# Kernel tuning notes

Measured on AMD Instinct MI355X. Metric: run time of the kernel, lower is better.

Reference implementation:

```python
import jax, jax.numpy as jnp
import numpy as np

LMBDA = 0.1
ALPHA = 0.05
NBIT = 4


def setup_inputs() -> dict:
    key = jax.random.key(0)
    k1, k2 = jax.random.split(key)
    shape = (4096, 16384)
    weight = jax.random.normal(k1, shape, dtype=jnp.float32) * 0.05
    Qn, Qp = -2 ** (NBIT - 1), 2 ** (NBIT - 1) - 1
    q_int = jax.random.randint(k2, shape, Qn, Qp + 1)  # bins in [-8, 7]
    weight_q = (q_int.astype(jnp.float32)) * ALPHA
    alpha = jnp.full((1,), ALPHA, dtype=jnp.float32)
    return {"weight": weight, "weight_q": weight_q, "nbit": NBIT, "alpha": alpha}


def reference(weight, weight_q, nbit, alpha):
    # dampening_loss with aggregation='mean', scaled by lmbda (single quant layer)
    Qn = -2 ** (nbit - 1)
    Qp = 2 ** (nbit - 1) - 1
    nbins = Qp - Qn + 1
    a = alpha.reshape(())

    # (w_q.detach() - w)^2 mean  (detach is a no-op in fwd)
    loss = jnp.mean((weight_q - weight) ** 2)

    # Fused histogram pass: per-bin count / sum / sumsq of `weight`,
    # keyed by the quant bin of weight_q (exact-equality mask in original).
    bin_id = jnp.round(weight_q / a).astype(jnp.int32) - Qn  # [0, nbins)
    w = weight.reshape(-1)
    b = bin_id.reshape(-1)
    cnt = jax.ops.segment_sum(jnp.ones_like(w), b, num_segments=nbins)
    s = jax.ops.segment_sum(w, b, num_segments=nbins)
    ss = jax.ops.segment_sum(w * w, b, num_segments=nbins)

    # unbiased variance per bin, only added when count > 1 (as in torch.var)
    denom_n = jnp.maximum(cnt, 1.0)
    denom_nm1 = jnp.maximum(cnt - 1.0, 1.0)
    var = (ss - s * s / denom_n) / denom_nm1
    loss = loss + jnp.sum(jnp.where(cnt > 1.0, var, 0.0))

    return LMBDA * loss
```

## Files before the change

kernel.cpp:

```cpp
#include <hip/hip_runtime.h>

#define NBINS  16
#define TPB    256
#define BLOCKS 768
#define PLANE  (NBINS * TPB)


__global__ __launch_bounds__(TPB) void binreg_main(
    const float* __restrict__ w, const float* __restrict__ wq,
    const float* __restrict__ alpha_p, const int* __restrict__ nbit_p,
    float* __restrict__ partial, long long n)
{
    __shared__ float  c_pl [PLANE];
    __shared__ float2 sv_pl[PLANE];
    __shared__ float  sqpart[TPB / 64];

    const int tid = threadIdx.x;

    #pragma unroll
    for (int k = 0; k < NBINS; ++k) {
        c_pl [k * TPB + tid] = 0.0f;
        sv_pl[k * TPB + tid] = make_float2(0.0f, 0.0f);
    }

    const float inv_a = 1.0f / alpha_p[0];
    const int   qoff  = 1 << (nbit_p[0] - 1);

    const long long n4     = n >> 2;
    const long long stride = (long long)BLOCKS * TPB;
    const float4* w4 = (const float4*)w;
    const float4* q4 = (const float4*)wq;

    float sq = 0.0f;

    for (long long i = (long long)blockIdx.x * TPB + tid; i < n4; i += stride) {
        float4 a = w4[i];
        float4 b = q4[i];

        float d0 = b.x - a.x, d1 = b.y - a.y, d2 = b.z - a.z, d3 = b.w - a.w;
        sq += d0 * d0 + d1 * d1 + d2 * d2 + d3 * d3;

        int i0 = ((((int)rintf(b.x * inv_a) + qoff) & (NBINS - 1)) << 8) + tid;
        int i1 = ((((int)rintf(b.y * inv_a) + qoff) & (NBINS - 1)) << 8) + tid;
        int i2 = ((((int)rintf(b.z * inv_a) + qoff) & (NBINS - 1)) << 8) + tid;
        int i3 = ((((int)rintf(b.w * inv_a) + qoff) & (NBINS - 1)) << 8) + tid;

        { c_pl[i0] += 1.0f; float2 t = sv_pl[i0]; t.x += a.x; t.y += a.x * a.x; sv_pl[i0] = t; }
        { c_pl[i1] += 1.0f; float2 t = sv_pl[i1]; t.x += a.y; t.y += a.y * a.y; sv_pl[i1] = t; }
        { c_pl[i2] += 1.0f; float2 t = sv_pl[i2]; t.x += a.z; t.y += a.z * a.z; sv_pl[i2] = t; }
        { c_pl[i3] += 1.0f; float2 t = sv_pl[i3]; t.x += a.w; t.y += a.w * a.w; sv_pl[i3] = t; }
    }

    for (long long i = (n4 << 2) + (long long)blockIdx.x * TPB + tid; i < n; i += stride) {
        float a = w[i], b = wq[i];
        float d = b - a;
        sq += d * d;
        int ii = ((((int)rintf(b * inv_a) + qoff) & (NBINS - 1)) << 8) + tid;
        c_pl[ii] += 1.0f; float2 t = sv_pl[ii]; t.x += a; t.y += a * a; sv_pl[ii] = t;
    }

    for (int off = 32; off; off >>= 1) sq += __shfl_down(sq, off, 64);
    const int wave = tid >> 6, lane = tid & 63;
    if (lane == 0) sqpart[wave] = sq;
    __syncthreads();

    for (int c = wave; c < 48; c += 4) {
        const int bin = c & 15;
        float v = 0.0f;
        if (c < 16) {
            #pragma unroll
            for (int r = 0; r < TPB / 64; ++r)
                v += c_pl[(bin << 8) + r * 64 + lane];
        } else if (c < 32) {
            #pragma unroll
            for (int r = 0; r < TPB / 64; ++r)
                v += sv_pl[(bin << 8) + r * 64 + lane].x;
        } else {
            #pragma unroll
            for (int r = 0; r < TPB / 64; ++r)
                v += sv_pl[(bin << 8) + r * 64 + lane].y;
        }
        for (int off = 32; off; off >>= 1) v += __shfl_down(v, off, 64);
        if (lane == 0) partial[c * BLOCKS + blockIdx.x] = v;
    }
    if (tid == 0)
        partial[48 * BLOCKS + blockIdx.x] =
            sqpart[0] + sqpart[1] + sqpart[2] + sqpart[3];
}

__global__ __launch_bounds__(TPB) void binreg_final(
    const float* __restrict__ partial, float* __restrict__ out, long long n)
{
    __shared__ float cell[49];
    const int tid = threadIdx.x, wave = tid >> 6, lane = tid & 63;

    for (int c = wave; c < 49; c += 4) {
        float v0 = 0.0f, v1 = 0.0f, v2 = 0.0f, v3 = 0.0f;
        for (int r = lane; r < BLOCKS; r += 256) {
            v0 += partial[c * BLOCKS + r];
            v1 += partial[c * BLOCKS + r + 64];
            v2 += partial[c * BLOCKS + r + 128];
            v3 += partial[c * BLOCKS + r + 192];
        }
        float v = (v0 + v1) + (v2 + v3);
        for (int off = 32; off; off >>= 1) v += __shfl_down(v, off, 64);
        if (lane == 0) cell[c] = v;
    }
    __syncthreads();

    if (tid == 0) {
        float loss = cell[48] / (float)n;
        #pragma unroll
        for (int b = 0; b < NBINS; ++b) {
            float cnt = cell[b];
            float s   = cell[16 + b];
            float ss  = cell[32 + b];
            if (cnt > 1.0f)
                loss += (ss - s * s / cnt) / (cnt - 1.0f);
        }
        out[0] = 0.1f * loss;
    }
}

extern "C" void kernel_launch(void* const* d_in, const int* in_sizes, int n_in,
                              void* d_out, int out_size, void* d_ws, size_t ws_size,
                              hipStream_t stream)
{
    const float* w     = (const float*)d_in[0];
    const float* wq    = (const float*)d_in[1];
    const int*   nbit  = (const int*)d_in[2];
    const float* alpha = (const float*)d_in[3];
    float* out     = (float*)d_out;
    float* partial = (float*)d_ws;
    long long n = (long long)in_sizes[0];

    binreg_main<<<BLOCKS, TPB, 0, stream>>>(w, wq, alpha, nbit, partial, n);
    binreg_final<<<1, TPB, 0, stream>>>(partial, out, n);
}
```

Measured before the change: 519.1 us.

## Count bins in packed register counters and merge duplicate bins before LDS updates

Per-bin counts move from a shared-memory plane into two 64-bit registers holding eight 8-bit counters each. These are flushed to float accumulators every 32 iterations and reduced across waves by shuffles. Within each float4, lanes that fall in the same bin are combined first, and duplicates are sent to a dummy LDS plane, so the four read-modify-writes never alias. The change also prefetches the next iteration's loads, raises the block count and adds an occupancy hint. It trades more VALU work and register pressure for less LDS traffic and shared-memory footprint.

```diff
diff --git a/kernel.cpp b/kernel.cpp
--- a/kernel.cpp
+++ b/kernel.cpp
@@ -2,26 +2,24 @@
 
 #define NBINS  16
 #define TPB    256
-#define BLOCKS 768
-#define PLANE  (NBINS * TPB)
-
-
-__global__ __launch_bounds__(TPB) void binreg_main(
+#define BLOCKS 1024
+#define DUMMY  16
+
+
+__global__ __launch_bounds__(TPB, 4) void binreg_main(
     const float* __restrict__ w, const float* __restrict__ wq,
     const float* __restrict__ alpha_p, const int* __restrict__ nbit_p,
     float* __restrict__ partial, long long n)
 {
-    __shared__ float  c_pl [PLANE];
-    __shared__ float2 sv_pl[PLANE];
+    __shared__ float2 sv_pl[(NBINS + 1) * TPB];
+    __shared__ float  cred[NBINS][TPB / 64];
     __shared__ float  sqpart[TPB / 64];
 
     const int tid = threadIdx.x;
 
     #pragma unroll
-    for (int k = 0; k < NBINS; ++k) {
-        c_pl [k * TPB + tid] = 0.0f;
+    for (int k = 0; k < NBINS; ++k)
         sv_pl[k * TPB + tid] = make_float2(0.0f, 0.0f);
-    }
 
     const float inv_a = 1.0f / alpha_p[0];
     const int   qoff  = 1 << (nbit_p[0] - 1);
@@ -32,46 +30,127 @@
     const float4* q4 = (const float4*)wq;
 
     float sq = 0.0f;
-
-    for (long long i = (long long)blockIdx.x * TPB + tid; i < n4; i += stride) {
+    unsigned long long clo = 0ull, chi = 0ull;
+    float cf[NBINS];
+    #pragma unroll
+    for (int k = 0; k < NBINS; ++k) cf[k] = 0.0f;
+    int pend = 0;
+
+    long long i = (long long)blockIdx.x * TPB + tid;
+    if (i < n4) {
         float4 a = w4[i];
         float4 b = q4[i];
-
-        float d0 = b.x - a.x, d1 = b.y - a.y, d2 = b.z - a.z, d3 = b.w - a.w;
-        sq += d0 * d0 + d1 * d1 + d2 * d2 + d3 * d3;
-
-        int i0 = ((((int)rintf(b.x * inv_a) + qoff) & (NBINS - 1)) << 8) + tid;
-        int i1 = ((((int)rintf(b.y * inv_a) + qoff) & (NBINS - 1)) << 8) + tid;
-        int i2 = ((((int)rintf(b.z * inv_a) + qoff) & (NBINS - 1)) << 8) + tid;
-        int i3 = ((((int)rintf(b.w * inv_a) + qoff) & (NBINS - 1)) << 8) + tid;
-
-        { c_pl[i0] += 1.0f; float2 t = sv_pl[i0]; t.x += a.x; t.y += a.x * a.x; sv_pl[i0] = t; }
-        { c_pl[i1] += 1.0f; float2 t = sv_pl[i1]; t.x += a.y; t.y += a.y * a.y; sv_pl[i1] = t; }
-        { c_pl[i2] += 1.0f; float2 t = sv_pl[i2]; t.x += a.z; t.y += a.z * a.z; sv_pl[i2] = t; }
-        { c_pl[i3] += 1.0f; float2 t = sv_pl[i3]; t.x += a.w; t.y += a.w * a.w; sv_pl[i3] = t; }
-    }
-
-    for (long long i = (n4 << 2) + (long long)blockIdx.x * TPB + tid; i < n; i += stride) {
-        float a = w[i], b = wq[i];
-        float d = b - a;
+        for (;;) {
+            const long long in  = i + stride;
+            const bool     more = in < n4;
+            float4 an, bn;
+            if (more) { an = w4[in]; bn = q4[in]; }
+
+            float d0 = b.x - a.x, d1 = b.y - a.y, d2 = b.z - a.z, d3 = b.w - a.w;
+            sq += d0 * d0 + d1 * d1 + d2 * d2 + d3 * d3;
+
+            const int b0 = (((int)rintf(b.x * inv_a)) + qoff) & (NBINS - 1);
+            const int b1 = (((int)rintf(b.y * inv_a)) + qoff) & (NBINS - 1);
+            const int b2 = (((int)rintf(b.z * inv_a)) + qoff) & (NBINS - 1);
+            const int b3 = (((int)rintf(b.w * inv_a)) + qoff) & (NBINS - 1);
+
+            {
+                unsigned long long t;
+                t = 1ull << ((b0 & 7) << 3); clo += (b0 < 8) ? t : 0ull; chi += (b0 < 8) ? 0ull : t;
+                t = 1ull << ((b1 & 7) << 3); clo += (b1 < 8) ? t : 0ull; chi += (b1 < 8) ? 0ull : t;
+                t = 1ull << ((b2 & 7) << 3); clo += (b2 < 8) ? t : 0ull; chi += (b2 < 8) ? 0ull : t;
+                t = 1ull << ((b3 & 7) << 3); clo += (b3 < 8) ? t : 0ull; chi += (b3 < 8) ? 0ull : t;
+            }
+
+            const bool e10 = (b1 == b0);
+            const bool e20 = (b2 == b0);
+            const bool e21 = (b2 == b1) && !e20;
+            const bool e30 = (b3 == b0);
+            const bool e31 = (b3 == b1) && !e30;
+            const bool e32 = (b3 == b2) && !e30 && !e31;
+
+            float sx0 = a.x, sx1 = a.y, sx2 = a.z, sx3 = a.w;
+            float qx0 = a.x * a.x, qx1 = a.y * a.y, qx2 = a.z * a.z, qx3 = a.w * a.w;
+
+            sx0 += e10 ? sx1 : 0.0f;  qx0 += e10 ? qx1 : 0.0f;
+            sx0 += e20 ? sx2 : 0.0f;  qx0 += e20 ? qx2 : 0.0f;
+            sx1 += e21 ? sx2 : 0.0f;  qx1 += e21 ? qx2 : 0.0f;
+            sx0 += e30 ? sx3 : 0.0f;  qx0 += e30 ? qx3 : 0.0f;
+            sx1 += e31 ? sx3 : 0.0f;  qx1 += e31 ? qx3 : 0.0f;
+            sx2 += e32 ? sx3 : 0.0f;  qx2 += e32 ? qx3 : 0.0f;
+
+            const int r1 = e10               ? DUMMY : b1;
+            const int r2 = (e20 | e21)       ? DUMMY : b2;
+            const int r3 = (e30 | e31 | e32) ? DUMMY : b3;
+            const int a0 = (b0 << 8) + tid;
+            const int a1 = (r1 << 8) + tid;
+            const int a2 = (r2 << 8) + tid;
+            const int a3 = (r3 << 8) + tid;
+
+            float2 t0 = sv_pl[a0];
+            float2 t1 = sv_pl[a1];
+            float2 t2 = sv_pl[a2];
+            float2 t3 = sv_pl[a3];
+            t0.x += sx0; t0.y += qx0;
+            t1.x += sx1; t1.y += qx1;
+            t2.x += sx2; t2.y += qx2;
+            t3.x += sx3; t3.y += qx3;
+            sv_pl[a0] = t0;
+            sv_pl[a1] = t1;
+            sv_pl[a2] = t2;
+            sv_pl[a3] = t3;
+
+            if (++pend >= 32) {
+                #pragma unroll
+                for (int k = 0; k < 8; ++k) {
+                    cf[k]     += (float)((clo >> (k * 8)) & 0xffull);
+                    cf[k + 8] += (float)((chi >> (k * 8)) & 0xffull);
+                }
+                clo = 0ull; chi = 0ull; pend = 0;
+            }
+
+            if (!more) break;
+            a = an; b = bn; i = in;
+        }
+    }
+
+    for (long long t = (n4 << 2) + (long long)blockIdx.x * TPB + tid; t < n; t += stride) {
+        float av = w[t], bv = wq[t];
+        float d = bv - av;
         sq += d * d;
-        int ii = ((((int)rintf(b * inv_a) + qoff) & (NBINS - 1)) << 8) + tid;
-        c_pl[ii] += 1.0f; float2 t = sv_pl[ii]; t.x += a; t.y += a * a; sv_pl[ii] = t;
+        int bb = (((int)rintf(bv * inv_a)) + qoff) & (NBINS - 1);
+        unsigned long long one = 1ull << ((bb & 7) << 3);
+        clo += (bb < 8) ? one : 0ull; chi += (bb < 8) ? 0ull : one;
+        int aa = (bb << 8) + tid;
+        float2 tt = sv_pl[aa]; tt.x += av; tt.y += av * av; sv_pl[aa] = tt;
+    }
+
+    #pragma unroll
+    for (int k = 0; k < 8; ++k) {
+        cf[k]     += (float)((clo >> (k * 8)) & 0xffull);
+        cf[k + 8] += (float)((chi >> (k * 8)) & 0xffull);
     }
 
     for (int off = 32; off; off >>= 1) sq += __shfl_down(sq, off, 64);
     const int wave = tid >> 6, lane = tid & 63;
     if (lane == 0) sqpart[wave] = sq;
+
+    #pragma unroll
+    for (int k = 0; k < NBINS; ++k) {
+        float v = cf[k];
+        for (int off = 32; off; off >>= 1) v += __shfl_down(v, off, 64);
+        if (lane == 0) cred[k][wave] = v;
+    }
     __syncthreads();
 
-    for (int c = wave; c < 48; c += 4) {
+    if (tid < NBINS)
+        partial[tid * BLOCKS + blockIdx.x] =
+            cred[tid][0] + cred[tid][1] + cred[tid][2] + cred[tid][3];
+
+    for (int c = 16 + wave; c < 48; c += 4) {
         const int bin = c & 15;
         float v = 0.0f;
-        if (c < 16) {
-            #pragma unroll
-            for (int r = 0; r < TPB / 64; ++r)
-                v += c_pl[(bin << 8) + r * 64 + lane];
-        } else if (c < 32) {
+        if (c < 32) {
             #pragma unroll
             for (int r = 0; r < TPB / 64; ++r)
                 v += sv_pl[(bin << 8) + r * 64 + lane].x;
```

Result: no change. 526.7 us (+1.5%).
